# Optimization experiments

Measured on AMD Instinct MI355X. Metric: run time of the kernel, lower is better.

## Reference

```python
import jax, jax.numpy as jnp
from jax import lax
import numpy as np

VOCAB = 8000
HIDDEN = 256
BATCH = 32
SEQ = 256


def setup_inputs() -> dict:
    key = jax.random.key(0)
    ks = jax.random.split(key, 8)
    s = 1.0 / np.sqrt(HIDDEN).astype(np.float32)  # torch nn.RNN / Linear init bound
    u = lambda k, shape: jax.random.uniform(k, shape, jnp.float32, -s, s)
    return {
        "X": jax.random.randint(ks[0], (BATCH, SEQ), 0, VOCAB),
        "h0": jnp.zeros((1, BATCH, HIDDEN), jnp.float32),
        "W_ih": u(ks[1], (HIDDEN, VOCAB)),   # rnn.weight_ih_l0
        "b_ih": u(ks[2], (HIDDEN,)),
        "W_hh": u(ks[3], (HIDDEN, HIDDEN)),  # rnn.weight_hh_l0
        "b_hh": u(ks[4], (HIDDEN,)),
        "W_out": u(ks[5], (VOCAB, HIDDEN)),  # dense.weight
        "b_out": u(ks[6], (VOCAB,)),
    }


def reference(X, h0, W_ih, b_ih, W_hh, b_hh, W_out, b_out):
    # one_hot(X) @ W_ih^T == gather of W_ih columns (same math, no dense one-hot)
    emb = W_ih.T[X]                              # (batch, seq, hidden)
    xp = jnp.transpose(emb, (1, 0, 2)) + b_ih    # (seq, batch, hidden)

    def step(h, x_t):
        h_new = jnp.tanh(x_t + h @ W_hh.T + b_hh)  # Elman cell, tanh nonlinearity
        return h_new, h_new

    h_last, Y = lax.scan(step, h0[0], xp)        # Y: (seq, batch, hidden)
    out = Y.reshape(-1, HIDDEN) @ W_out.T + b_out  # (seq*batch, vocab)
    return out, h_last[None]
```

## Files before the change

kernel.cpp:

```cpp
#include <hip/hip_runtime.h>
#include <hip/hip_bf16.h>

#define VOCAB 8000
#define HIDDEN 256
#define BATCH 32
#define SEQ 256
#define NPAD 8064
#define MROWS (SEQ * BATCH)

typedef __attribute__((ext_vector_type(8))) short short8;
typedef __attribute__((ext_vector_type(4))) short short4v;
typedef __attribute__((ext_vector_type(4))) float floatx4;


__device__ __forceinline__ void async_copy16(const void* g, void* l) {
    __builtin_amdgcn_global_load_lds(
        (const __attribute__((address_space(1))) unsigned int*)g,
        (__attribute__((address_space(3))) unsigned int*)l, 16, 0, 0);
}

__device__ __forceinline__ unsigned short f32_to_bf16(float f) {
    unsigned int u = __float_as_uint(f);
    unsigned int lsb = (u >> 16) & 1u;
    u += 0x7fffu + lsb;
    return (unsigned short)(u >> 16);
}

__device__ __forceinline__ float bf16_to_f32(unsigned short u) {
    return __uint_as_float(((unsigned int)u) << 16);
}


__global__ void __launch_bounds__(256) convw_kernel(const float* __restrict__ W_out,
                                                    unsigned short* __restrict__ Wbf) {
    int v = blockIdx.x;
    int k = threadIdx.x;
    float f = (v < VOCAB) ? W_out[(size_t)v * HIDDEN + k] : 0.0f;
    Wbf[(size_t)v * HIDDEN + k] = f32_to_bf16(f);
}


__global__ void __launch_bounds__(256) gather_kernel(const int* __restrict__ X,
                                                     const float* __restrict__ W_ih,
                                                     const float* __restrict__ b_ih,
                                                     float* __restrict__ xp) {
    int n = blockIdx.x;
    int h = threadIdx.x;
    int s = n >> 5;
    int b = n & 31;
    int tok = X[b * SEQ + s];
    xp[(size_t)n * HIDDEN + h] = W_ih[(size_t)h * VOCAB + tok] + b_ih[h];
}


#define HSTR 264

__global__ void __launch_bounds__(512, 2) rnn_kernel(const float* __restrict__ xp,
                                                     const float* __restrict__ h0,
                                                     const float* __restrict__ W_hh,
                                                     const float* __restrict__ b_hh,
                                                     unsigned short* __restrict__ Ybf,
                                                     float* __restrict__ h_last) {
    __shared__ __align__(16) unsigned short Hh[2][16 * HSTR];

    const int tid  = threadIdx.x;
    const int lane = tid & 63;
    const int w    = tid >> 6;
    const int l16  = lane & 15;
    const int lq   = lane >> 4;
    const int bg0  = blockIdx.x * 16;

    short8 Whi[2][8], Wlo[2][8];
#pragma unroll
    for (int t = 0; t < 2; ++t) {
#pragma unroll
        for (int c = 0; c < 8; ++c) {
            const float* p = W_hh + (size_t)(32 * w + 16 * t + l16) * HIDDEN + 32 * c + 8 * lq;
            float4 f0 = *(const float4*)p;
            float4 f1 = *(const float4*)(p + 4);
            float v[8] = {f0.x, f0.y, f0.z, f0.w, f1.x, f1.y, f1.z, f1.w};
            short8 hi, lo;
#pragma unroll
            for (int e = 0; e < 8; ++e) {
                unsigned short h16 = f32_to_bf16(v[e]);
                hi[e] = (short)h16;
                lo[e] = (short)f32_to_bf16(v[e] - bf16_to_f32(h16));
            }
            Whi[t][c] = hi;
            Wlo[t][c] = lo;
        }
    }

    float4 bhh[2];
#pragma unroll
    for (int t = 0; t < 2; ++t)
        bhh[t] = *(const float4*)(b_hh + 32 * w + 16 * t + 4 * lq);

    {
        int b  = tid >> 5;
        int k0 = (tid & 31) * 8;
#pragma unroll
        for (int k = 0; k < 8; ++k)
            Hh[0][b * HSTR + k0 + k] = f32_to_bf16(h0[(size_t)(bg0 + b) * HIDDEN + k0 + k]);
    }

    float4 xbuf[2];
#pragma unroll
    for (int t = 0; t < 2; ++t)
        xbuf[t] = *(const float4*)(xp + (size_t)(bg0 + l16) * HIDDEN + 32 * w + 16 * t + 4 * lq);

    __syncthreads();

#pragma unroll 1
    for (int s = 0; s < SEQ; ++s) {
        const unsigned short* Hc = Hh[s & 1];
        unsigned short*       Hn = Hh[(s & 1) ^ 1];

        short8 hb[8];
#pragma unroll
        for (int c = 0; c < 8; ++c)
            hb[c] = *(const short8*)&Hc[l16 * HSTR + 32 * c + 8 * lq];

        floatx4 a1[2], a2[2];
#pragma unroll
        for (int t = 0; t < 2; ++t) {
            a1[t][0] = xbuf[t].x + bhh[t].x;
            a1[t][1] = xbuf[t].y + bhh[t].y;
            a1[t][2] = xbuf[t].z + bhh[t].z;
            a1[t][3] = xbuf[t].w + bhh[t].w;
            a2[t][0] = a2[t][1] = a2[t][2] = a2[t][3] = 0.f;
        }

        if (s + 1 < SEQ) {
#pragma unroll
            for (int t = 0; t < 2; ++t)
                xbuf[t] = *(const float4*)(xp + (size_t)((s + 1) * BATCH + bg0 + l16) * HIDDEN +
                                           32 * w + 16 * t + 4 * lq);
        }

#pragma unroll
        for (int c = 0; c < 8; ++c) {
            a1[0] = __builtin_amdgcn_mfma_f32_16x16x32_bf16(Whi[0][c], hb[c], a1[0], 0, 0, 0);
            a1[1] = __builtin_amdgcn_mfma_f32_16x16x32_bf16(Whi[1][c], hb[c], a1[1], 0, 0, 0);
            a2[0] = __builtin_amdgcn_mfma_f32_16x16x32_bf16(Wlo[0][c], hb[c], a2[0], 0, 0, 0);
            a2[1] = __builtin_amdgcn_mfma_f32_16x16x32_bf16(Wlo[1][c], hb[c], a2[1], 0, 0, 0);
        }

#pragma unroll
        for (int t = 0; t < 2; ++t) {
            const int i0 = 32 * w + 16 * t + 4 * lq;
            float hn[4];
            short4v hi4;
#pragma unroll
            for (int r = 0; r < 4; ++r) {
                float a  = a1[t][r] + a2[t][r];
                float e  = __builtin_amdgcn_exp2f(a * 2.88539004f);
                float rc = __builtin_amdgcn_rcpf(e + 1.0f);
                hn[r] = fmaf(-2.0f, rc, 1.0f);
                hi4[r] = (short)f32_to_bf16(hn[r]);
            }
            *(short4v*)&Hn[l16 * HSTR + i0] = hi4;
            *(short4v*)(Ybf + (size_t)(s * BATCH + bg0 + l16) * HIDDEN + i0) = hi4;
            if (s == SEQ - 1) {
#pragma unroll
                for (int r = 0; r < 4; ++r)
                    h_last[(size_t)(bg0 + l16) * HIDDEN + i0 + r] = hn[r];
            }
        }
        __syncthreads();
    }
}


__global__ void __launch_bounds__(256) gemm_kernel(const unsigned short* __restrict__ Ybf,
                                                   const unsigned short* __restrict__ Wbf,
                                                   const float* __restrict__ b_out,
                                                   float* __restrict__ out) {
    __shared__ __align__(16) short sA[128 * 32];
    __shared__ __align__(16) short sB[128 * 32];

    const int tid  = threadIdx.x;
    const int lane = tid & 63;
    const int wave = tid >> 6;
    const int wm   = wave >> 1;
    const int wn   = wave & 1;
    const int l16  = lane & 15;
    const int lq   = lane >> 4;

    const int m0 = blockIdx.y * 128;
    const int n0 = blockIdx.x * 128;

    floatx4 acc[4][4] = {};

    const int chunk0 = tid;
    const int chunk1 = 256 + tid;
    const int rowA0 = chunk0 >> 2, kc0 = chunk0 & 3;
    const int rowA1 = chunk1 >> 2, kc1 = chunk1 & 3;

    for (int k0 = 0; k0 < HIDDEN; k0 += 32) {
        async_copy16(Ybf + (size_t)(m0 + rowA0) * HIDDEN + k0 + kc0 * 8, sA + chunk0 * 8);
        async_copy16(Ybf + (size_t)(m0 + rowA1) * HIDDEN + k0 + kc1 * 8, sA + chunk1 * 8);
        async_copy16(Wbf + (size_t)(n0 + rowA0) * HIDDEN + k0 + kc0 * 8, sB + chunk0 * 8);
        async_copy16(Wbf + (size_t)(n0 + rowA1) * HIDDEN + k0 + kc1 * 8, sB + chunk1 * 8);
        __syncthreads();

        short8 afrag[4], bfrag[4];
#pragma unroll
        for (int t = 0; t < 4; ++t) {
            afrag[t] = *(const short8*)&sA[(wm * 64 + t * 16 + l16) * 32 + lq * 8];
            bfrag[t] = *(const short8*)&sB[(wn * 64 + t * 16 + l16) * 32 + lq * 8];
        }
#pragma unroll
        for (int tm = 0; tm < 4; ++tm)
#pragma unroll
            for (int tn = 0; tn < 4; ++tn)
                acc[tm][tn] = __builtin_amdgcn_mfma_f32_16x16x32_bf16(
                    afrag[tm], bfrag[tn], acc[tm][tn], 0, 0, 0);
        __syncthreads();
    }

#pragma unroll
    for (int tn = 0; tn < 4; ++tn) {
        int n = n0 + wn * 64 + tn * 16 + l16;
        if (n < VOCAB) {
            float bo = b_out[n];
#pragma unroll
            for (int tm = 0; tm < 4; ++tm) {
                int mbase = m0 + wm * 64 + tm * 16 + lq * 4;
#pragma unroll
                for (int r = 0; r < 4; ++r) {
                    out[(size_t)(mbase + r) * VOCAB + n] = acc[tm][tn][r] + bo;
                }
            }
        }
    }
}


extern "C" void kernel_launch(void* const* d_in, const int* in_sizes, int n_in,
                              void* d_out, int out_size, void* d_ws, size_t ws_size,
                              hipStream_t stream) {
    const int*   X     = (const int*)d_in[0];
    const float* h0    = (const float*)d_in[1];
    const float* W_ih  = (const float*)d_in[2];
    const float* b_ih  = (const float*)d_in[3];
    const float* W_hh  = (const float*)d_in[4];
    const float* b_hh  = (const float*)d_in[5];
    const float* W_out = (const float*)d_in[6];
    const float* b_out = (const float*)d_in[7];

    float* out    = (float*)d_out;
    float* h_last = out + (size_t)MROWS * VOCAB;

    char* ws = (char*)d_ws;
    float*          xp  = (float*)ws;
    unsigned short* Ybf = (unsigned short*)(ws + 8388608);
    unsigned short* Wbf = (unsigned short*)(ws + 41943040);

    hipLaunchKernelGGL(convw_kernel,  dim3(NPAD),        dim3(256), 0, stream, W_out, Wbf);
    hipLaunchKernelGGL(gather_kernel, dim3(SEQ * BATCH), dim3(256), 0, stream, X, W_ih, b_ih, xp);
    hipLaunchKernelGGL(rnn_kernel,    dim3(2),           dim3(512), 0, stream,
                       xp, h0, W_hh, b_hh, Ybf, h_last);
    hipLaunchKernelGGL(gemm_kernel,   dim3(NPAD / 128, MROWS / 128), dim3(256), 0, stream,
                       Ybf, Wbf, b_out, out);
}
```

Measured before the change: 637.9 us.

## Fuse RNN recurrence and output GEMM into one persistent producer-consumer kernel

Merges the sequential RNN and the vocab-projection GEMM into one persistent kernel. Two blocks run the recurrence and publish progress through a global atomic counter every 8 steps. The other 126 blocks spin-wait on that counter and compute 128x256 output tiles as soon as the rows they need are ready, so the GEMM overlaps the latency-bound recurrence. The embedding gather is replaced by a pre-transposed W_ih that the RNN reads directly by token, and the convert and transpose work is merged into one prep kernel. This risks deadlock if the producer blocks are not co-resident with the consumers, and it adds spin-wait overhead.

New measurement: 597.0 us. 6.4% less time.

```diff
diff --git a/kernel.cpp b/kernel.cpp
--- a/kernel.cpp
+++ b/kernel.cpp
@@ -1,12 +1,16 @@
 #include <hip/hip_runtime.h>
-#include <hip/hip_bf16.h>
 
 #define VOCAB 8000
 #define HIDDEN 256
 #define BATCH 32
 #define SEQ 256
-#define NPAD 8064
+#define NPAD 8192
 #define MROWS (SEQ * BATCH)
+#define HSTR 264
+#define NCONS 126
+#define TM_TILES (MROWS / 128)
+#define TN_TILES (NPAD / 256)
+#define TRB 2000
 
 typedef __attribute__((ext_vector_type(8))) short short8;
 typedef __attribute__((ext_vector_type(4))) short short4v;
@@ -31,37 +35,46 @@
 }
 
 
-__global__ void __launch_bounds__(256) convw_kernel(const float* __restrict__ W_out,
-                                                    unsigned short* __restrict__ Wbf) {
-    int v = blockIdx.x;
-    int k = threadIdx.x;
-    float f = (v < VOCAB) ? W_out[(size_t)v * HIDDEN + k] : 0.0f;
-    Wbf[(size_t)v * HIDDEN + k] = f32_to_bf16(f);
-}
-
-
-__global__ void __launch_bounds__(256) gather_kernel(const int* __restrict__ X,
-                                                     const float* __restrict__ W_ih,
-                                                     const float* __restrict__ b_ih,
-                                                     float* __restrict__ xp) {
-    int n = blockIdx.x;
-    int h = threadIdx.x;
-    int s = n >> 5;
-    int b = n & 31;
-    int tok = X[b * SEQ + s];
-    xp[(size_t)n * HIDDEN + h] = W_ih[(size_t)h * VOCAB + tok] + b_ih[h];
-}
-
-
-#define HSTR 264
-
-__global__ void __launch_bounds__(512, 2) rnn_kernel(const float* __restrict__ xp,
-                                                     const float* __restrict__ h0,
-                                                     const float* __restrict__ W_hh,
-                                                     const float* __restrict__ b_hh,
-                                                     unsigned short* __restrict__ Ybf,
-                                                     float* __restrict__ h_last) {
-    __shared__ __align__(16) unsigned short Hh[2][16 * HSTR];
+__global__ void __launch_bounds__(256) prep_kernel(const float* __restrict__ W_ih,
+                                                   float* __restrict__ W_ihT,
+                                                   const float* __restrict__ W_out,
+                                                   unsigned short* __restrict__ Wbf,
+                                                   int* __restrict__ progress) {
+    const int bid = blockIdx.x;
+    if (bid < TRB) {
+        if (bid == 0 && threadIdx.x == 0) *progress = 0;
+        __shared__ float tile[32][33];
+        const int tv = (bid % 250) * 32;
+        const int th = (bid / 250) * 32;
+        const int tx = threadIdx.x & 31;
+        const int ty = threadIdx.x >> 5;
+#pragma unroll
+        for (int k = 0; k < 4; ++k)
+            tile[ty + 8 * k][tx] = W_ih[(size_t)(th + ty + 8 * k) * VOCAB + tv + tx];
+        __syncthreads();
+#pragma unroll
+        for (int k = 0; k < 4; ++k)
+            W_ihT[(size_t)(tv + ty + 8 * k) * HIDDEN + th + tx] = tile[tx][ty + 8 * k];
+    } else {
+        const int v = bid - TRB;
+        const int k = threadIdx.x;
+        float f = (v < VOCAB) ? W_out[(size_t)v * HIDDEN + k] : 0.0f;
+        Wbf[(size_t)v * HIDDEN + k] = f32_to_bf16(f);
+    }
+}
+
+
+__device__ __forceinline__ void rnn_role(const float* __restrict__ W_ihT,
+                                         const int* __restrict__ X,
+                                         const float* __restrict__ h0,
+                                         const float* __restrict__ W_hh,
+                                         const float* __restrict__ b_hh,
+                                         const float* __restrict__ b_ih,
+                                         unsigned short* __restrict__ Ybf,
+                                         float* __restrict__ h_last,
+                                         int* __restrict__ progress,
+                                         char* smem) {
+    unsigned short (*Hh)[16 * HSTR] = (unsigned short (*)[16 * HSTR])smem;
 
     const int tid  = threadIdx.x;
     const int lane = tid & 63;
@@ -93,8 +106,12 @@
 
     float4 bhh[2];
 #pragma unroll
-    for (int t = 0; t < 2; ++t)
-        bhh[t] = *(const float4*)(b_hh + 32 * w + 16 * t + 4 * lq);
+    for (int t = 0; t < 2; ++t) {
+        float4 a = *(const float4*)(b_hh + 32 * w + 16 * t + 4 * lq);
+        float4 b = *(const float4*)(b_ih + 32 * w + 16 * t + 4 * lq);
+        bhh[t].x = a.x + b.x; bhh[t].y = a.y + b.y;
+        bhh[t].z = a.z + b.z; bhh[t].w = a.w + b.w;
+    }
 
     {
         int b  = tid >> 5;
@@ -104,10 +121,14 @@
             Hh[0][b * HSTR + k0 + k] = f32_to_bf16(h0[(size_t)(bg0 + b) * HIDDEN + k0 + k]);
     }
 
+    const int xrow = (bg0 + l16) * SEQ;
     float4 xbuf[2];
-#pragma unroll
-    for (int t = 0; t < 2; ++t)
-        xbuf[t] = *(const float4*)(xp + (size_t)(bg0 + l16) * HIDDEN + 32 * w + 16 * t + 4 * lq);
+    {
+        int tok = X[xrow];
+#pragma unroll
+        for (int t = 0; t < 2; ++t)
+            xbuf[t] = *(const float4*)(W_ihT + (size_t)tok * HIDDEN + 32 * w + 16 * t + 4 * lq);
+    }
 
     __syncthreads();
 
@@ -132,10 +153,10 @@
         }
 
         if (s + 1 < SEQ) {
+            int tok = X[xrow + s + 1];
 #pragma unroll
             for (int t = 0; t < 2; ++t)
-                xbuf[t] = *(const float4*)(xp + (size_t)((s + 1) * BATCH + bg0 + l16) * HIDDEN +
-                                           32 * w + 16 * t + 4 * lq);
+                xbuf[t] = *(const float4*)(W_ihT + (size_t)tok * HIDDEN + 32 * w + 16 * t + 4 * lq);
         }
 
 #pragma unroll
@@ -168,72 +189,111 @@
             }
         }
         __syncthreads();
-    }
-}
-
-
-__global__ void __launch_bounds__(256) gemm_kernel(const unsigned short* __restrict__ Ybf,
-                                                   const unsigned short* __restrict__ Wbf,
-                                                   const float* __restrict__ b_out,
-                                                   float* __restrict__ out) {
-    __shared__ __align__(16) short sA[128 * 32];
-    __shared__ __align__(16) short sB[128 * 32];
+
+        if (((s & 7) == 7) && tid == 0)
+            __hip_atomic_fetch_add(progress, 1, __ATOMIC_RELEASE, __HIP_MEMORY_SCOPE_AGENT);
+    }
+}
+
+__device__ __forceinline__ void gemm_role(const unsigned short* __restrict__ Ybf,
+                                          const unsigned short* __restrict__ Wbf,
+                                          const float* __restrict__ b_out,
+                                          float* __restrict__ out,
+                                          int* __restrict__ progress,
+                                          char* smem) {
+    short* sA = (short*)smem;
+    short* sB = (short*)(smem + 128 * 32 * 2);
 
     const int tid  = threadIdx.x;
     const int lane = tid & 63;
     const int wave = tid >> 6;
-    const int wm   = wave >> 1;
-    const int wn   = wave & 1;
+    const int wm   = wave >> 2;
+    const int wn   = wave & 3;
     const int l16  = lane & 15;
     const int lq   = lane >> 4;
-
-    const int m0 = blockIdx.y * 128;
-    const int n0 = blockIdx.x * 128;
-
-    floatx4 acc[4][4] = {};
-
-    const int chunk0 = tid;
-    const int chunk1 = 256 + tid;
-    const int rowA0 = chunk0 >> 2, kc0 = chunk0 & 3;
-    const int rowA1 = chunk1 >> 2, kc1 = chunk1 & 3;
-
-    for (int k0 = 0; k0 < HIDDEN; k0 += 32) {
-        async_copy16(Ybf + (size_t)(m0 + rowA0) * HIDDEN + k0 + kc0 * 8, sA + chunk0 * 8);
-        async_copy16(Ybf + (size_t)(m0 + rowA1) * HIDDEN + k0 + kc1 * 8, sA + chunk1 * 8);
-        async_copy16(Wbf + (size_t)(n0 + rowA0) * HIDDEN + k0 + kc0 * 8, sB + chunk0 * 8);
-        async_copy16(Wbf + (size_t)(n0 + rowA1) * HIDDEN + k0 + kc1 * 8, sB + chunk1 * 8);
+    const int cid  = blockIdx.x - 2;
+
+    int fenced = 0;
+
+    for (int T = cid; T < TM_TILES * TN_TILES; T += NCONS) {
+        const int tm = T >> 5;
+        const int tn = T & 31;
+        const int m0 = tm * 128;
+        const int n0 = tn * 256;
+
+        if (tid == 0) {
+            const int need = 2 * ((tm >> 1) + 1);
+            if (need > fenced) {
+                while (__hip_atomic_load(progress, __ATOMIC_RELAXED, __HIP_MEMORY_SCOPE_AGENT) < need)
+                    __builtin_amdgcn_s_sleep(8);
+                __builtin_amdgcn_fence(__ATOMIC_ACQUIRE, "agent");
+                fenced = need;
+            }
+        }
         __syncthreads();
 
-        short8 afrag[4], bfrag[4];
-#pragma unroll
-        for (int t = 0; t < 4; ++t) {
-            afrag[t] = *(const short8*)&sA[(wm * 64 + t * 16 + l16) * 32 + lq * 8];
-            bfrag[t] = *(const short8*)&sB[(wn * 64 + t * 16 + l16) * 32 + lq * 8];
-        }
-#pragma unroll
-        for (int tm = 0; tm < 4; ++tm)
-#pragma unroll
-            for (int tn = 0; tn < 4; ++tn)
-                acc[tm][tn] = __builtin_amdgcn_mfma_f32_16x16x32_bf16(
-                    afrag[tm], bfrag[tn], acc[tm][tn], 0, 0, 0);
-        __syncthreads();
-    }
-
-#pragma unroll
-    for (int tn = 0; tn < 4; ++tn) {
-        int n = n0 + wn * 64 + tn * 16 + l16;
-        if (n < VOCAB) {
-            float bo = b_out[n];
-#pragma unroll
-            for (int tm = 0; tm < 4; ++tm) {
-                int mbase = m0 + wm * 64 + tm * 16 + lq * 4;
-#pragma unroll
-                for (int r = 0; r < 4; ++r) {
-                    out[(size_t)(mbase + r) * VOCAB + n] = acc[tm][tn][r] + bo;
+        floatx4 acc[4][4] = {};
+
+        const int rA  = tid >> 2, kcA = tid & 3;
+        const int c1  = tid + 512;
+        const int rB1 = c1 >> 2,  kB1 = c1 & 3;
+
+        for (int k0 = 0; k0 < HIDDEN; k0 += 32) {
+            async_copy16(Ybf + (size_t)(m0 + rA) * HIDDEN + k0 + kcA * 8, sA + tid * 8);
+            async_copy16(Wbf + (size_t)(n0 + rA) * HIDDEN + k0 + kcA * 8, sB + tid * 8);
+            async_copy16(Wbf + (size_t)(n0 + rB1) * HIDDEN + k0 + kB1 * 8, sB + c1 * 8);
+            __syncthreads();
+
+            short8 af[4], bfr[4];
+#pragma unroll
+            for (int t = 0; t < 4; ++t) {
+                af[t]  = *(const short8*)&sA[(wm * 64 + t * 16 + l16) * 32 + lq * 8];
+                bfr[t] = *(const short8*)&sB[(wn * 64 + t * 16 + l16) * 32 + lq * 8];
+            }
+#pragma unroll
+            for (int a = 0; a < 4; ++a)
+#pragma unroll
+                for (int b = 0; b < 4; ++b)
+                    acc[a][b] = __builtin_amdgcn_mfma_f32_16x16x32_bf16(
+                        af[a], bfr[b], acc[a][b], 0, 0, 0);
+            __syncthreads();
+        }
+
+#pragma unroll
+        for (int tn4 = 0; tn4 < 4; ++tn4) {
+            int n = n0 + wn * 64 + tn4 * 16 + l16;
+            if (n < VOCAB) {
+                float bo = b_out[n];
+#pragma unroll
+                for (int tm4 = 0; tm4 < 4; ++tm4) {
+                    int mbase = m0 + wm * 64 + tm4 * 16 + lq * 4;
+#pragma unroll
+                    for (int r = 0; r < 4; ++r)
+                        __builtin_nontemporal_store(acc[tm4][tn4][r] + bo,
+                            &out[(size_t)(mbase + r) * VOCAB + n]);
                 }
             }
         }
     }
+}
+
+__global__ void __launch_bounds__(512, 2) fused_kernel(const float* __restrict__ W_ihT,
+                                                       const int* __restrict__ X,
+                                                       const float* __restrict__ h0,
+                                                       const float* __restrict__ W_hh,
+                                                       const float* __restrict__ b_hh,
+                                                       const float* __restrict__ b_ih,
+                                                       unsigned short* __restrict__ Ybf,
+                                                       float* __restrict__ h_last,
+                                                       const unsigned short* __restrict__ Wbf,
+                                                       const float* __restrict__ b_out,
+                                                       float* __restrict__ out,
+                                                       int* __restrict__ progress) {
+    __shared__ __align__(16) char smem[24576];
+    if (blockIdx.x < 2)
+        rnn_role(W_ihT, X, h0, W_hh, b_hh, b_ih, Ybf, h_last, progress, smem);
+    else
+        gemm_role(Ybf, Wbf, b_out, out, progress, smem);
 }
 
 
@@ -253,14 +313,13 @@
     float* h_last = out + (size_t)MROWS * VOCAB;
 
     char* ws = (char*)d_ws;
-    float*          xp  = (float*)ws;
-    unsigned short* Ybf = (unsigned short*)(ws + 8388608);
-    unsigned short* Wbf = (unsigned short*)(ws + 41943040);
-
-    hipLaunchKernelGGL(convw_kernel,  dim3(NPAD),        dim3(256), 0, stream, W_out, Wbf);
-    hipLaunchKernelGGL(gather_kernel, dim3(SEQ * BATCH), dim3(256), 0, stream, X, W_ih, b_ih, xp);
-    hipLaunchKernelGGL(rnn_kernel,    dim3(2),           dim3(512), 0, stream,
-                       xp, h0, W_hh, b_hh, Ybf, h_last);
-    hipLaunchKernelGGL(gemm_kernel,   dim3(NPAD / 128, MROWS / 128), dim3(256), 0, stream,
-                       Ybf, Wbf, b_out, out);
-}
+    float*          W_ihT    = (float*)ws;
+    unsigned short* Ybf      = (unsigned short*)(ws + 8192000);
+    unsigned short* Wbf      = (unsigned short*)(ws + 12386304);
+    int*            progress = (int*)(ws + 16580608);
+
+    hipLaunchKernelGGL(prep_kernel, dim3(TRB + NPAD), dim3(256), 0, stream,
+                       W_ih, W_ihT, W_out, Wbf, progress);
+    hipLaunchKernelGGL(fused_kernel, dim3(2 + NCONS), dim3(512), 0, stream,
+                       W_ihT, X, h0, W_hh, b_hh, b_ih, Ybf, h_last, Wbf, b_out, out, progress);
+}
```
